# Kernel tuning notes

Measured on AMD Instinct MI355X. Metric: run time of the kernel, lower is better.

## Reference

```python
import jax, jax.numpy as jnp
import numpy as np

T_MEDIA = 3      # torch.arange(3)
N_LATENTS = 64   # repeat(..., m=64)
H = 8            # rearrange h=8
D_HEAD = 64


def setup_inputs() -> dict:
    key = jax.random.key(0)
    ks = jax.random.split(key, 6)
    B, S = 4, 2048
    Dv, Dt = 2048, 4096
    inner = H * D_HEAD  # 512
    latent = jax.random.normal(ks[0], (B, T_MEDIA, N_LATENTS, Dv), dtype=jnp.float32)
    y = jax.random.normal(ks[1], (B, S, Dt), dtype=jnp.float32)
    media_mask = jax.random.randint(ks[2], (B, S), 0, T_MEDIA + 1)  # values in {0,1,2,3}
    W_vk = jax.random.normal(ks[3], (Dv, 2 * inner), dtype=jnp.float32) / np.sqrt(Dv)
    W_q = jax.random.normal(ks[4], (Dt, inner), dtype=jnp.float32) / np.sqrt(Dt)
    W_out = jax.random.normal(ks[5], (inner, Dt), dtype=jnp.float32) / np.sqrt(inner)
    return {"latent": latent, "y": y, "media_mask": media_mask,
            "W_vk": W_vk, "W_q": W_q, "W_out": W_out}


def reference(latent, y, media_mask, W_vk, W_q, W_out):
    B, T, N, Dv = latent.shape
    S = y.shape[1]
    # b t n d -> b (t n) d
    vf = latent.reshape(B, T * N, Dv)
    kv = vf @ W_vk                      # [B, TN, 2*H*Dh]
    k, v = jnp.split(kv, 2, axis=-1)
    q = y @ W_q                         # [B, S, H*Dh]
    def to_heads(x):
        b, n, _ = x.shape
        return x.reshape(b, n, H, D_HEAD).transpose(0, 2, 1, 3)  # b h n d
    q, k, v = to_heads(q), to_heads(k), to_heads(v)
    # NOTE: original applies no 1/sqrt(d) scaling (self.temp unused)
    sim = jnp.einsum('bhid,bhjd->bhij', q, k)   # [B, H, S, T*N]
    media_time = jnp.arange(T) + 1                               # [T]
    key_time = jnp.repeat(media_time, N)                         # [T*N]
    t2m = media_mask[:, None, :, None] == key_time[None, None, None, :]
    neg = -jnp.finfo(sim.dtype).max
    sim = jnp.where(t2m, sim, neg)
    logits = jax.nn.softmax(sim, axis=-1)
    no_media = (media_mask == 0)[:, None, :, None]
    logits = jnp.where(no_media, 0.0, logits)
    out = jnp.einsum('bhij,bhjd->bhid', logits, v)               # [B, H, S, Dh]
    out = out.transpose(0, 2, 1, 3).reshape(B, S, H * D_HEAD)
    return out @ W_out
```

## Files before the change

### kernel.cpp

```cpp
#include <hip/hip_runtime.h>
#include <hip/hip_bf16.h>

typedef __attribute__((ext_vector_type(4))) float f32x4;
typedef __attribute__((ext_vector_type(8))) short bf16x8;
typedef __attribute__((ext_vector_type(8))) unsigned short u16x8;

#define QCAP 8256
#define QSTR ((size_t)QCAP * 512)
#define KVB 48

__device__ __forceinline__ unsigned short f2bf(float f) {
  unsigned int u = __builtin_bit_cast(unsigned int, f);
  unsigned int r = (u + 0x7FFFu + ((u >> 16) & 1u)) >> 16;
  return (unsigned short)r;
}
__device__ __forceinline__ float bf2f(unsigned short h) {
  unsigned int u = ((unsigned int)h) << 16;
  return __builtin_bit_cast(float, u);
}

__device__ __forceinline__ void gload_lds16(const void* g, void* l) {
  __builtin_amdgcn_global_load_lds(
      (__attribute__((address_space(1))) unsigned int*)g,
      (__attribute__((address_space(3))) unsigned int*)l, 16, 0, 0);
}

__global__ __launch_bounds__(1024) void gather_scan(
    const int* __restrict__ mask, int* __restrict__ offs,
    int* __restrict__ glob, int* __restrict__ mcnt, int* __restrict__ mlist) {
  __shared__ int scnt[13];
  __shared__ int so[13];
  int tid = threadIdx.x;
  if (tid < 13) scnt[tid] = 0;
  __syncthreads();
#pragma unroll
  for (int i = 0; i < 8; ++i) {
    int g = i * 1024 + tid;
    int m = mask[g];
    atomicAdd(&scnt[m > 0 ? (g >> 11) * 3 + m - 1 : 12], 1);
  }
  __syncthreads();
  if (tid == 0) {
    int s = 0;
#pragma unroll
    for (int i = 0; i < 12; ++i) {
      so[i] = s;
      s += scnt[i];
    }
    so[12] = s;
#pragma unroll
    for (int i = 0; i < 13; ++i) offs[i] = so[i];
    *mcnt = scnt[12];
  }
  __syncthreads();
  if (tid < 13) scnt[tid] = 0;
  __syncthreads();
#pragma unroll
  for (int i = 0; i < 8; ++i) {
    int g = i * 1024 + tid;
    int m = mask[g];
    if (m > 0) {
      int bt = (g >> 11) * 3 + m - 1;
      int p = atomicAdd(&scnt[bt], 1);
      glob[so[bt] + p] = g;
    } else {
      int p = atomicAdd(&scnt[12], 1);
      mlist[p] = g;
    }
  }
}

__global__ __launch_bounds__(256) void prep_all(
    const float* __restrict__ y, const int* __restrict__ glob,
    const int* __restrict__ offs, unsigned short* __restrict__ ybf,
    const float* __restrict__ Wq, const float* __restrict__ Wvk,
    const float* __restrict__ Wo, const float* __restrict__ latent,
    unsigned short* __restrict__ QTh, unsigned short* __restrict__ VKh,
    unsigned short* __restrict__ VKl, unsigned short* __restrict__ OTh,
    unsigned short* __restrict__ latbf) {
  int bid = blockIdx.x;
  if (bid < 16384) {
    int p = bid >> 1, half = bid & 1;
    if (p >= offs[12]) return;
    int g = glob[p];
    const float* src = y + (size_t)g * 4096 + half * 2048 + threadIdx.x * 8;
    unsigned short* dst = ybf + (size_t)p * 4096 + half * 2048 + threadIdx.x * 8;
    f32x4 a = *(const f32x4*)src;
    f32x4 b = *(const f32x4*)(src + 4);
    u16x8 o;
#pragma unroll
    for (int j = 0; j < 4; ++j) o[j] = f2bf(a[j]);
#pragma unroll
    for (int j = 0; j < 4; ++j) o[4 + j] = f2bf(b[j]);
    *(u16x8*)dst = o;
    return;
  }
  if (bid >= 22528) {
    long i = ((long)(bid - 22528) * 256 + threadIdx.x) * 8;
    f32x4 a = *(const f32x4*)(latent + i);
    f32x4 b = *(const f32x4*)(latent + i + 4);
    u16x8 o;
#pragma unroll
    for (int j = 0; j < 4; ++j) o[j] = f2bf(a[j]);
#pragma unroll
    for (int j = 0; j < 4; ++j) o[4 + j] = f2bf(b[j]);
    *(u16x8*)(latbf + i) = o;
    return;
  }
  int wb = bid - 16384;
  __shared__ float tile[32][33];
  const float* W;
  unsigned short *Th, *Tl;
  int K, N, nbx, b;
  if (wb < 2048) {
    W = Wq; Th = QTh; Tl = nullptr; K = 4096; N = 512; nbx = 16; b = wb;
  } else if (wb < 4096) {
    W = Wvk; Th = VKh; Tl = VKl; K = 2048; N = 1024; nbx = 32; b = wb - 2048;
  } else {
    W = Wo; Th = OTh; Tl = nullptr; K = 512; N = 4096; nbx = 128; b = wb - 4096;
  }
  int n0 = (b % nbx) * 32, k0 = (b / nbx) * 32;
  int tx = threadIdx.x & 31, ty = threadIdx.x >> 5;
#pragma unroll
  for (int r = 0; r < 4; ++r)
    tile[ty + 8 * r][tx] = W[(size_t)(k0 + ty + 8 * r) * N + n0 + tx];
  __syncthreads();
#pragma unroll
  for (int r = 0; r < 4; ++r) {
    float f = tile[tx][ty + 8 * r];
    unsigned short hi = f2bf(f);
    size_t o = (size_t)(n0 + ty + 8 * r) * K + k0 + tx;
    Th[o] = hi;
    if (Tl) Tl[o] = f2bf(f - bf2f(hi));
  }
}

#define BM 128
#define BN 128
#define BK 64

__global__ __launch_bounds__(256) void gemm_dual(
    const unsigned short* __restrict__ latbf, const unsigned short* __restrict__ VKh,
    const unsigned short* __restrict__ VKl, const unsigned short* __restrict__ ybf,
    const unsigned short* __restrict__ QTh, unsigned short* __restrict__ Kh,
    unsigned short* __restrict__ Kl, unsigned short* __restrict__ Vt,
    float* __restrict__ qc, const int* __restrict__ offs) {
  __shared__ unsigned short smem[BM * BK + BN * BK + 64];
  unsigned short* Ald = smem;
  unsigned short* Bhld = smem + BM * BK;
  float* epi = (float*)smem;

  int tid = threadIdx.x, lane = tid & 63, wid = tid >> 6;
  int wr = wid >> 1, wc = wid & 1;
  bool isKV = blockIdx.x < KVB;
  const unsigned short* Ab;
  const unsigned short* Bb = nullptr;
  int K, kbeg, kend, bm, bn, ks = 0;
  if (isKV) {
    int sw = (blockIdx.x & 7) * (KVB >> 3) + (blockIdx.x >> 3);
    bm = sw / 8;
    bn = sw % 8;
    Ab = latbf + (size_t)(bm * BM) * 2048;
    K = 2048;
    kbeg = 0;
    kend = 2048;
  } else {
    int qb = blockIdx.x - KVB;
    int w = (qb & 7) * 64 + (qb >> 3);
    bm = w & 63;
    int r = w >> 6;
    bn = r >> 1;
    ks = r & 1;
    if (bm * BM >= offs[12]) return;
    Ab = ybf + (size_t)(bm * BM) * 4096;
    Bb = QTh + (size_t)(bn * BN) * 4096;
    K = 4096;
    kbeg = ks * 2048;
    kend = kbeg + 2048;
  }

  int fr = lane & 15, fq = lane >> 4;
  int srow = lane >> 3, scol = ((lane & 7) ^ (lane >> 3)) * 8;

  f32x4 acc[4][4];
#pragma unroll
  for (int i = 0; i < 4; ++i)
#pragma unroll
    for (int j = 0; j < 4; ++j) acc[i][j] = (f32x4){0.f, 0.f, 0.f, 0.f};

  int npass = isKV ? 2 : 1;
#pragma unroll 1
  for (int pass = 0; pass < npass; ++pass) {
    const unsigned short* Bp =
        isKV ? ((pass ? VKl : VKh) + (size_t)(bn * BN) * 2048) : Bb;
    for (int k0 = kbeg; k0 < kend; k0 += BK) {
#pragma unroll
      for (int i = 0; i < 4; ++i) {
        int c = wid * 4 + i;
        size_t go = (size_t)(c * 8 + srow) * K + k0 + scol;
        gload_lds16(Ab + go, &Ald[c * 512]);
        gload_lds16(Bp + go, &Bhld[c * 512]);
      }
      __syncthreads();
#pragma unroll
      for (int kk = 0; kk < 2; ++kk) {
        int ca = (kk * 32 + fq * 8) ^ ((fr & 7) * 8);
        bf16x8 af[4], bf[4];
#pragma unroll
        for (int i = 0; i < 4; ++i) {
          af[i] = *(const bf16x8*)&Ald[(wr * 64 + i * 16 + fr) * BK + ca];
          bf[i] = *(const bf16x8*)&Bhld[(wc * 64 + i * 16 + fr) * BK + ca];
        }
#pragma unroll
        for (int mi = 0; mi < 4; ++mi)
#pragma unroll
          for (int ni = 0; ni < 4; ++ni)
            acc[mi][ni] = __builtin_amdgcn_mfma_f32_16x16x32_bf16(
                af[mi], bf[ni], acc[mi][ni], 0, 0, 0);
      }
      __syncthreads();
    }
  }

  if (isKV) {
#pragma unroll
    for (int mi = 0; mi < 4; ++mi)
#pragma unroll
      for (int ni = 0; ni < 4; ++ni)
#pragma unroll
        for (int r = 0; r < 4; ++r) {
          int row = bm * BM + wr * 64 + mi * 16 + fq * 4 + r;
          int col = bn * BN + wc * 64 + ni * 16 + fr;
          int bt = row >> 6, key = row & 63;
          float v = acc[mi][ni][r];
          if (col < 512) {
            int h = col >> 6, d = col & 63;
            unsigned short hi = f2bf(v);
            size_t o = ((size_t)(bt * 8 + h) * 64 + key) * 64 + d;
            Kh[o] = hi;
            Kl[o] = f2bf(v - bf2f(hi));
          } else {
            int c = col - 512;
            int h = c >> 6, d = c & 63;
            Vt[((size_t)(bt * 8 + h) * 64 + d) * 64 + key] = f2bf(v);
          }
        }
    return;
  }

#pragma unroll 1
  for (int p = 0; p < 2; ++p) {
    __syncthreads();
    if (wr == p) {
#pragma unroll
      for (int mi = 0; mi < 4; ++mi)
#pragma unroll
        for (int ni = 0; ni < 4; ++ni)
#pragma unroll
          for (int r = 0; r < 4; ++r) {
            int lrow = mi * 16 + fq * 4 + r;
            int lcol = wc * 64 + ni * 16 + fr;
            int pc = lcol ^ ((lrow & 7) << 4);
            epi[lrow * 128 + pc] = acc[mi][ni][r];
          }
    }
    __syncthreads();
#pragma unroll
    for (int k = 0; k < 8; ++k) {
      int chunk = k * 256 + tid;
      int lrow = chunk >> 5;
      int c4 = (chunk & 31) * 4;
      int pc4 = c4 ^ ((lrow & 7) << 4);
      f32x4 v = *(f32x4*)&epi[lrow * 128 + pc4];
      int row = bm * BM + p * 64 + lrow;
      *(f32x4*)&qc[(size_t)ks * QSTR + (size_t)row * 512 + bn * BN + c4] = v;
    }
  }
}

__global__ __launch_bounds__(256) void gemm_out(
    const unsigned short* __restrict__ A, const unsigned short* __restrict__ Bh,
    float* __restrict__ Cv, const int* __restrict__ glob,
    const int* __restrict__ offs, const int* __restrict__ mcnt,
    const int* __restrict__ mlist, int M, int N, int K) {
  __shared__ unsigned short smem[BM * BK + BN * BK + 64];
  unsigned short* Ald = smem;
  unsigned short* Bhld = smem + BM * BK;
  float* epi = (float*)smem;

  int tid = threadIdx.x, lane = tid & 63, wid = tid >> 6;
  int wr = wid >> 1, wc = wid & 1;
  int nwg = gridDim.x;
  int w = (blockIdx.x & 7) * (nwg >> 3) + (blockIdx.x >> 3);
  int nTN = N / BN;
  int nBM = M / BM;
  int bm = w % nBM;
  int bn = w / nBM;
  int mv = offs[12];

  if (bm * BM >= mv) {
    int bmLive = (mv + BM - 1) / BM;
    int nDead = (nBM - bmLive) * nTN;
    int deadIdx = (bm - bmLive) + bn * (nBM - bmLive);
    int nm = *mcnt;
    f32x4 z = (f32x4){0.f, 0.f, 0.f, 0.f};
    for (int j = deadIdx; j < nm; j += nDead) {
      float* row = Cv + (size_t)mlist[j] * N;
#pragma unroll
      for (int i = 0; i < 4; ++i) *(f32x4*)&row[(i * 256 + tid) * 4] = z;
    }
    return;
  }

  const unsigned short* Ab = A + (size_t)(bm * BM) * K;
  const unsigned short* Bhb = Bh + (size_t)(bn * BN) * K;
  int fr = lane & 15, fq = lane >> 4;
  int srow = lane >> 3, scol = ((lane & 7) ^ (lane >> 3)) * 8;

  f32x4 acc[4][4];
#pragma unroll
  for (int i = 0; i < 4; ++i)
#pragma unroll
    for (int j = 0; j < 4; ++j) acc[i][j] = (f32x4){0.f, 0.f, 0.f, 0.f};

  for (int k0 = 0; k0 < K; k0 += BK) {
#pragma unroll
    for (int i = 0; i < 4; ++i) {
      int c = wid * 4 + i;
      size_t go = (size_t)(c * 8 + srow) * K + k0 + scol;
      gload_lds16(Ab + go, &Ald[c * 512]);
      gload_lds16(Bhb + go, &Bhld[c * 512]);
    }
    __syncthreads();
#pragma unroll
    for (int kk = 0; kk < 2; ++kk) {
      int ca = (kk * 32 + fq * 8) ^ ((fr & 7) * 8);
      bf16x8 af[4], bf[4];
#pragma unroll
      for (int i = 0; i < 4; ++i) {
        af[i] = *(const bf16x8*)&Ald[(wr * 64 + i * 16 + fr) * BK + ca];
        bf[i] = *(const bf16x8*)&Bhld[(wc * 64 + i * 16 + fr) * BK + ca];
      }
#pragma unroll
      for (int mi = 0; mi < 4; ++mi)
#pragma unroll
        for (int ni = 0; ni < 4; ++ni)
          acc[mi][ni] = __builtin_amdgcn_mfma_f32_16x16x32_bf16(
              af[mi], bf[ni], acc[mi][ni], 0, 0, 0);
    }
    __syncthreads();
  }

#pragma unroll 1
  for (int p = 0; p < 2; ++p) {
    __syncthreads();
    if (wr == p) {
#pragma unroll
      for (int mi = 0; mi < 4; ++mi)
#pragma unroll
        for (int ni = 0; ni < 4; ++ni)
#pragma unroll
          for (int r = 0; r < 4; ++r) {
            int lrow = mi * 16 + fq * 4 + r;
            int lcol = wc * 64 + ni * 16 + fr;
            int pc = lcol ^ ((lrow & 7) << 4);
            epi[lrow * 128 + pc] = acc[mi][ni][r];
          }
    }
    __syncthreads();
#pragma unroll
    for (int k = 0; k < 8; ++k) {
      int chunk = k * 256 + tid;
      int lrow = chunk >> 5;
      int c4 = (chunk & 31) * 4;
      int pc4 = c4 ^ ((lrow & 7) << 4);
      f32x4 v = *(f32x4*)&epi[lrow * 128 + pc4];
      int row = bm * BM + p * 64 + lrow;
      if (row < mv)
        *(f32x4*)&Cv[(size_t)glob[row] * N + bn * BN + c4] = v;
    }
  }

  int bmLive = (mv + BM - 1) / BM;
  if (bmLive == nBM && bm == 0) {
    int nm = *mcnt;
    f32x4 z = (f32x4){0.f, 0.f, 0.f, 0.f};
    for (int j = bn; j < nm; j += nTN) {
      float* row = Cv + (size_t)mlist[j] * N;
#pragma unroll
      for (int i = 0; i < 4; ++i) *(f32x4*)&row[(i * 256 + tid) * 4] = z;
    }
  }
}

__global__ __launch_bounds__(256) void attn5(
    const float* __restrict__ qc, const unsigned short* __restrict__ Kh,
    const unsigned short* __restrict__ Kl, const unsigned short* __restrict__ Vt,
    const int* __restrict__ offs, unsigned short* __restrict__ attnc) {
  __shared__ unsigned short Pl[4][32][72];
  int tid = threadIdx.x, wid = tid >> 6, lane = tid & 63;
  int fr = lane & 15, fq = lane >> 4;
  int bt = blockIdx.x >> 6, rt = blockIdx.x & 63;
  int n = offs[bt + 1] - offs[bt];
  int rbase = rt * 32;
  if (rbase >= n) return;
  int qbase = offs[bt] + rbase;

#pragma unroll 1
  for (int hp = 0; hp < 2; ++hp) {
    int h = wid * 2 + hp;
    const unsigned short* khb = Kh + ((size_t)(bt * 8 + h) * 64) * 64;
    const unsigned short* klb = Kl + ((size_t)(bt * 8 + h) * 64) * 64;
    const unsigned short* vtb = Vt + ((size_t)(bt * 8 + h) * 64) * 64;

    f32x4 sacc[2][4];
#pragma unroll
    for (int i = 0; i < 2; ++i)
#pragma unroll
      for (int j = 0; j < 4; ++j) sacc[i][j] = (f32x4){0.f, 0.f, 0.f, 0.f};

#pragma unroll
    for (int kk = 0; kk < 2; ++kk) {
      bf16x8 qh[2], ql[2];
#pragma unroll
      for (int mi = 0; mi < 2; ++mi) {
        size_t qo = (size_t)(qbase + mi * 16 + fr) * 512 + h * 64 + kk * 32 + fq * 8;
        f32x4 s0 = *(const f32x4*)(qc + qo) + *(const f32x4*)(qc + QSTR + qo);
        f32x4 s1 = *(const f32x4*)(qc + qo + 4) +
                   *(const f32x4*)(qc + QSTR + qo + 4);
        float sv[8];
        *(f32x4*)&sv[0] = s0;
        *(f32x4*)&sv[4] = s1;
#pragma unroll
        for (int j = 0; j < 8; ++j) {
          unsigned short hi = f2bf(sv[j]);
          qh[mi][j] = (short)hi;
          ql[mi][j] = (short)f2bf(sv[j] - bf2f(hi));
        }
      }
#pragma unroll
      for (int ni = 0; ni < 4; ++ni) {
        size_t ko = (size_t)(ni * 16 + fr) * 64 + kk * 32 + fq * 8;
        bf16x8 kh = *(const bf16x8*)(khb + ko);
        bf16x8 kl = *(const bf16x8*)(klb + ko);
#pragma unroll
        for (int mi = 0; mi < 2; ++mi) {
          sacc[mi][ni] = __builtin_amdgcn_mfma_f32_16x16x32_bf16(
              qh[mi], kh, sacc[mi][ni], 0, 0, 0);
          sacc[mi][ni] = __builtin_amdgcn_mfma_f32_16x16x32_bf16(
              qh[mi], kl, sacc[mi][ni], 0, 0, 0);
          sacc[mi][ni] = __builtin_amdgcn_mfma_f32_16x16x32_bf16(
              ql[mi], kh, sacc[mi][ni], 0, 0, 0);
        }
      }
    }

#pragma unroll
    for (int mi = 0; mi < 2; ++mi) {
#pragma unroll
      for (int r = 0; r < 4; ++r) {
        float m = fmaxf(fmaxf(sacc[mi][0][r], sacc[mi][1][r]),
                        fmaxf(sacc[mi][2][r], sacc[mi][3][r]));
#pragma unroll
        for (int o = 1; o < 16; o <<= 1) m = fmaxf(m, __shfl_xor(m, o));
        float e0 = __expf(sacc[mi][0][r] - m);
        float e1 = __expf(sacc[mi][1][r] - m);
        float e2 = __expf(sacc[mi][2][r] - m);
        float e3 = __expf(sacc[mi][3][r] - m);
        float s = e0 + e1 + e2 + e3;
#pragma unroll
        for (int o = 1; o < 16; o <<= 1) s += __shfl_xor(s, o);
        float inv = 1.f / s;
        int row = mi * 16 + fq * 4 + r;
        Pl[wid][row][fr] = f2bf(e0 * inv);
        Pl[wid][row][16 + fr] = f2bf(e1 * inv);
        Pl[wid][row][32 + fr] = f2bf(e2 * inv);
        Pl[wid][row][48 + fr] = f2bf(e3 * inv);
      }
    }

    f32x4 oacc[2][4];
#pragma unroll
    for (int i = 0; i < 2; ++i)
#pragma unroll
      for (int j = 0; j < 4; ++j) oacc[i][j] = (f32x4){0.f, 0.f, 0.f, 0.f};
#pragma unroll
    for (int kk = 0; kk < 2; ++kk) {
      bf16x8 pa[2];
#pragma unroll
      for (int mi = 0; mi < 2; ++mi)
        pa[mi] = *(const bf16x8*)&Pl[wid][mi * 16 + fr][kk * 32 + fq * 8];
#pragma unroll
      for (int ni = 0; ni < 4; ++ni) {
        bf16x8 vb = *(const bf16x8*)(vtb + (size_t)(ni * 16 + fr) * 64 +
                                     kk * 32 + fq * 8);
#pragma unroll
        for (int mi = 0; mi < 2; ++mi)
          oacc[mi][ni] = __builtin_amdgcn_mfma_f32_16x16x32_bf16(
              pa[mi], vb, oacc[mi][ni], 0, 0, 0);
      }
    }

#pragma unroll
    for (int mi = 0; mi < 2; ++mi)
#pragma unroll
      for (int r = 0; r < 4; ++r) {
        int row = mi * 16 + fq * 4 + r;
        if (rbase + row < n) {
          unsigned short* ar = attnc + (size_t)(qbase + row) * 512 + h * 64 + fr;
          ar[0] = f2bf(oacc[mi][0][r]);
          ar[16] = f2bf(oacc[mi][1][r]);
          ar[32] = f2bf(oacc[mi][2][r]);
          ar[48] = f2bf(oacc[mi][3][r]);
        }
      }
  }
}

extern "C" void kernel_launch(void* const* d_in, const int* in_sizes, int n_in,
                              void* d_out, int out_size, void* d_ws,
                              size_t ws_size, hipStream_t stream) {
  const float* latent = (const float*)d_in[0];
  const float* y = (const float*)d_in[1];
  const int* mask = (const int*)d_in[2];
  const float* W_vk = (const float*)d_in[3];
  const float* W_q = (const float*)d_in[4];
  const float* W_out = (const float*)d_in[5];
  float* out = (float*)d_out;

  char* ws = (char*)d_ws;
  size_t off = 0;
  auto alloc = [&](size_t bytes) -> void* {
    void* p = ws + off;
    off = (off + bytes + 255) & ~(size_t)255;
    return p;
  };
  unsigned short* WqT_h = (unsigned short*)alloc((size_t)512 * 4096 * 2);
  unsigned short* WvkT_h = (unsigned short*)alloc((size_t)1024 * 2048 * 2);
  unsigned short* WvkT_l = (unsigned short*)alloc((size_t)1024 * 2048 * 2);
  unsigned short* WoT_h = (unsigned short*)alloc((size_t)4096 * 512 * 2);
  unsigned short* ybf = (unsigned short*)alloc((size_t)8192 * 4096 * 2);
  unsigned short* latbf = (unsigned short*)alloc((size_t)768 * 2048 * 2);
  float* qc = (float*)alloc((size_t)2 * QCAP * 512 * 4);
  unsigned short* Khb = (unsigned short*)alloc((size_t)768 * 512 * 2);
  unsigned short* Klb = (unsigned short*)alloc((size_t)768 * 512 * 2);
  unsigned short* Vtb = (unsigned short*)alloc((size_t)768 * 512 * 2);
  unsigned short* attnc = (unsigned short*)alloc((size_t)8192 * 512 * 2);
  int* offs = (int*)alloc(13 * 4);
  int* glob = (int*)alloc(8192 * 4);
  int* mcnt = (int*)alloc(4);
  int* mlist = (int*)alloc(8192 * 4);

  gather_scan<<<1, 1024, 0, stream>>>(mask, offs, glob, mcnt, mlist);

  prep_all<<<23296, 256, 0, stream>>>(y, glob, offs, ybf, W_q, W_vk, W_out,
                                      latent, WqT_h, WvkT_h, WvkT_l, WoT_h,
                                      latbf);

  gemm_dual<<<KVB + 512, 256, 0, stream>>>(latbf, WvkT_h, WvkT_l, ybf, WqT_h,
                                           Khb, Klb, Vtb, qc, offs);
  attn5<<<12 * 64, 256, 0, stream>>>(qc, Khb, Klb, Vtb, offs, attnc);
  gemm_out<<<(8192 / BM) * (4096 / BN), 256, 0, stream>>>(
      attnc, WoT_h, out, glob, offs, mcnt, mlist, 8192, 4096, 512);
}
```

Measured before the change: 211.8 us.

## Double-buffer LDS tiles with async prefetch in both GEMM kernels

Both GEMM kernels now keep two LDS buffers and issue the global-to-LDS loads for the next K step before computing on the current one, waiting with explicit vmcnt counts instead of a full drain. The KV path merges its two passes (hi and lo weights) into one flattened step loop so the prefetch runs across the pass boundary. This is meant to hide global load latency behind MFMA work, at the cost of doubled LDS per block, which may lower occupancy.

```diff
diff --git a/kernel.cpp b/kernel.cpp
--- a/kernel.cpp
+++ b/kernel.cpp
@@ -138,6 +138,7 @@
 #define BM 128
 #define BN 128
 #define BK 64
+#define BUFE (BM * BK + BN * BK)
 
 __global__ __launch_bounds__(256) void gemm_dual(
     const unsigned short* __restrict__ latbf, const unsigned short* __restrict__ VKh,
@@ -145,25 +146,27 @@
     const unsigned short* __restrict__ QTh, unsigned short* __restrict__ Kh,
     unsigned short* __restrict__ Kl, unsigned short* __restrict__ Vt,
     float* __restrict__ qc, const int* __restrict__ offs) {
-  __shared__ unsigned short smem[BM * BK + BN * BK + 64];
-  unsigned short* Ald = smem;
-  unsigned short* Bhld = smem + BM * BK;
+  __shared__ unsigned short smem[2 * BUFE + 64];
   float* epi = (float*)smem;
 
   int tid = threadIdx.x, lane = tid & 63, wid = tid >> 6;
   int wr = wid >> 1, wc = wid & 1;
   bool isKV = blockIdx.x < KVB;
   const unsigned short* Ab;
+  const unsigned short* VKhb = nullptr;
+  const unsigned short* VKlb = nullptr;
   const unsigned short* Bb = nullptr;
-  int K, kbeg, kend, bm, bn, ks = 0;
+  int K, kbeg, bm, bn, ks = 0, nsteps;
   if (isKV) {
     int sw = (blockIdx.x & 7) * (KVB >> 3) + (blockIdx.x >> 3);
     bm = sw / 8;
     bn = sw % 8;
     Ab = latbf + (size_t)(bm * BM) * 2048;
+    VKhb = VKh + (size_t)(bn * BN) * 2048;
+    VKlb = VKl + (size_t)(bn * BN) * 2048;
     K = 2048;
     kbeg = 0;
-    kend = 2048;
+    nsteps = 64;
   } else {
     int qb = blockIdx.x - KVB;
     int w = (qb & 7) * 64 + (qb >> 3);
@@ -176,50 +179,73 @@
     Bb = QTh + (size_t)(bn * BN) * 4096;
     K = 4096;
     kbeg = ks * 2048;
-    kend = kbeg + 2048;
+    nsteps = 32;
   }
 
   int fr = lane & 15, fq = lane >> 4;
   int srow = lane >> 3, scol = ((lane & 7) ^ (lane >> 3)) * 8;
 
+  auto stage = [&](int bufsel, int s) {
+    int k0;
+    const unsigned short* Bbase;
+    if (isKV) {
+      k0 = (s & 31) * BK;
+      Bbase = (s >= 32) ? VKlb : VKhb;
+    } else {
+      k0 = kbeg + s * BK;
+      Bbase = Bb;
+    }
+    unsigned short* Al = smem + bufsel * BUFE;
+    unsigned short* Bl2 = Al + BM * BK;
+#pragma unroll
+    for (int i = 0; i < 4; ++i) {
+      int c = wid * 4 + i;
+      size_t go = (size_t)(c * 8 + srow) * K + k0 + scol;
+      gload_lds16(Ab + go, &Al[c * 512]);
+      gload_lds16(Bbase + go, &Bl2[c * 512]);
+    }
+  };
+
   f32x4 acc[4][4];
 #pragma unroll
   for (int i = 0; i < 4; ++i)
 #pragma unroll
     for (int j = 0; j < 4; ++j) acc[i][j] = (f32x4){0.f, 0.f, 0.f, 0.f};
 
-  int npass = isKV ? 2 : 1;
+  stage(0, 0);
 #pragma unroll 1
-  for (int pass = 0; pass < npass; ++pass) {
-    const unsigned short* Bp =
-        isKV ? ((pass ? VKl : VKh) + (size_t)(bn * BN) * 2048) : Bb;
-    for (int k0 = kbeg; k0 < kend; k0 += BK) {
+  for (int s = 0; s < nsteps; ++s) {
+    int cur = s & 1;
+    if (s + 1 < nsteps) {
+      stage(1 - cur, s + 1);
+      asm volatile("s_waitcnt vmcnt(8)" ::: "memory");
+    } else {
+      asm volatile("s_waitcnt vmcnt(0)" ::: "memory");
+    }
+    __builtin_amdgcn_sched_barrier(0);
+    __builtin_amdgcn_s_barrier();
+    __builtin_amdgcn_sched_barrier(0);
+    const unsigned short* Al = smem + cur * BUFE;
+    const unsigned short* Bl2 = Al + BM * BK;
+#pragma unroll
+    for (int kk = 0; kk < 2; ++kk) {
+      int ca = (kk * 32 + fq * 8) ^ ((fr & 7) * 8);
+      bf16x8 af[4], bf[4];
 #pragma unroll
       for (int i = 0; i < 4; ++i) {
-        int c = wid * 4 + i;
-        size_t go = (size_t)(c * 8 + srow) * K + k0 + scol;
-        gload_lds16(Ab + go, &Ald[c * 512]);
-        gload_lds16(Bp + go, &Bhld[c * 512]);
+        af[i] = *(const bf16x8*)&Al[(wr * 64 + i * 16 + fr) * BK + ca];
+        bf[i] = *(const bf16x8*)&Bl2[(wc * 64 + i * 16 + fr) * BK + ca];
       }
-      __syncthreads();
-#pragma unroll
-      for (int kk = 0; kk < 2; ++kk) {
-        int ca = (kk * 32 + fq * 8) ^ ((fr & 7) * 8);
-        bf16x8 af[4], bf[4];
-#pragma unroll
-        for (int i = 0; i < 4; ++i) {
-          af[i] = *(const bf16x8*)&Ald[(wr * 64 + i * 16 + fr) * BK + ca];
-          bf[i] = *(const bf16x8*)&Bhld[(wc * 64 + i * 16 + fr) * BK + ca];
-        }
-#pragma unroll
-        for (int mi = 0; mi < 4; ++mi)
-#pragma unroll
-          for (int ni = 0; ni < 4; ++ni)
-            acc[mi][ni] = __builtin_amdgcn_mfma_f32_16x16x32_bf16(
-                af[mi], bf[ni], acc[mi][ni], 0, 0, 0);
-      }
-      __syncthreads();
-    }
+#pragma unroll
+      for (int mi = 0; mi < 4; ++mi)
+#pragma unroll
+        for (int ni = 0; ni < 4; ++ni)
+          acc[mi][ni] = __builtin_amdgcn_mfma_f32_16x16x32_bf16(
+              af[mi], bf[ni], acc[mi][ni], 0, 0, 0);
+    }
+    __builtin_amdgcn_sched_barrier(0);
+    __builtin_amdgcn_s_barrier();
+    __builtin_amdgcn_sched_barrier(0);
   }
 
   if (isKV) {
@@ -283,9 +309,7 @@
     float* __restrict__ Cv, const int* __restrict__ glob,
     const int* __restrict__ offs, const int* __restrict__ mcnt,
     const int* __restrict__ mlist, int M, int N, int K) {
-  __shared__ unsigned short smem[BM * BK + BN * BK + 64];
-  unsigned short* Ald = smem;
-  unsigned short* Bhld = smem + BM * BK;
+  __shared__ unsigned short smem[2 * BUFE + 64];
   float* epi = (float*)smem;
 
   int tid = threadIdx.x, lane = tid & 63, wid = tid >> 6;
@@ -316,30 +340,50 @@
   const unsigned short* Bhb = Bh + (size_t)(bn * BN) * K;
   int fr = lane & 15, fq = lane >> 4;
   int srow = lane >> 3, scol = ((lane & 7) ^ (lane >> 3)) * 8;
-
-  f32x4 acc[4][4];
-#pragma unroll
-  for (int i = 0; i < 4; ++i)
-#pragma unroll
-    for (int j = 0; j < 4; ++j) acc[i][j] = (f32x4){0.f, 0.f, 0.f, 0.f};
-
-  for (int k0 = 0; k0 < K; k0 += BK) {
+  int nsteps = K / BK;
+
+  auto stage = [&](int bufsel, int s) {
+    int k0 = s * BK;
+    unsigned short* Al = smem + bufsel * BUFE;
+    unsigned short* Bl2 = Al + BM * BK;
 #pragma unroll
     for (int i = 0; i < 4; ++i) {
       int c = wid * 4 + i;
       size_t go = (size_t)(c * 8 + srow) * K + k0 + scol;
-      gload_lds16(Ab + go, &Ald[c * 512]);
-      gload_lds16(Bhb + go, &Bhld[c * 512]);
-    }
-    __syncthreads();
+      gload_lds16(Ab + go, &Al[c * 512]);
+      gload_lds16(Bhb + go, &Bl2[c * 512]);
+    }
+  };
+
+  f32x4 acc[4][4];
+#pragma unroll
+  for (int i = 0; i < 4; ++i)
+#pragma unroll
+    for (int j = 0; j < 4; ++j) acc[i][j] = (f32x4){0.f, 0.f, 0.f, 0.f};
+
+  stage(0, 0);
+#pragma unroll 1
+  for (int s = 0; s < nsteps; ++s) {
+    int cur = s & 1;
+    if (s + 1 < nsteps) {
+      stage(1 - cur, s + 1);
+      asm volatile("s_waitcnt vmcnt(8)" ::: "memory");
+    } else {
+      asm volatile("s_waitcnt vmcnt(0)" ::: "memory");
+    }
+    __builtin_amdgcn_sched_barrier(0);
+    __builtin_amdgcn_s_barrier();
+    __builtin_amdgcn_sched_barrier(0);
+    const unsigned short* Al = smem + cur * BUFE;
+    const unsigned short* Bl2 = Al + BM * BK;
 #pragma unroll
     for (int kk = 0; kk < 2; ++kk) {
       int ca = (kk * 32 + fq * 8) ^ ((fr & 7) * 8);
       bf16x8 af[4], bf[4];
 #pragma unroll
       for (int i = 0; i < 4; ++i) {
-        af[i] = *(const bf16x8*)&Ald[(wr * 64 + i * 16 + fr) * BK + ca];
-        bf[i] = *(const bf16x8*)&Bhld[(wc * 64 + i * 16 + fr) * BK + ca];
+        af[i] = *(const bf16x8*)&Al[(wr * 64 + i * 16 + fr) * BK + ca];
+        bf[i] = *(const bf16x8*)&Bl2[(wc * 64 + i * 16 + fr) * BK + ca];
       }
 #pragma unroll
       for (int mi = 0; mi < 4; ++mi)
@@ -348,7 +392,9 @@
           acc[mi][ni] = __builtin_amdgcn_mfma_f32_16x16x32_bf16(
               af[mi], bf[ni], acc[mi][ni], 0, 0, 0);
     }
-    __syncthreads();
+    __builtin_amdgcn_sched_barrier(0);
+    __builtin_amdgcn_s_barrier();
+    __builtin_amdgcn_sched_barrier(0);
   }
 
 #pragma unroll 1
```

Result: slower. 259.8 us (+22.7%).
